# Kernel tuning notes

Hardware: AMD Instinct MI355X
Metric: run time of the kernel (lower is better)

## Reference

```python
import jax, jax.numpy as jnp
import numpy as np

T, A = 2048, 64          # n_thread, n_agents
RAWOB, N_TP, N_GP = 120, 5, 2
E = N_TP * N_GP          # number of sub-nets (type x group placeholder)
D = RAWOB + N_TP + 1     # augmented obs dim fed to each Net
H = 128                  # hidden width of each sub-net MLP
N_ACTION = 16


def setup_inputs() -> dict:
    key = jax.random.key(0)
    ks = jax.random.split(key, 12)
    s1 = 1.0 / np.sqrt(D)
    s2 = 1.0 / np.sqrt(H)
    return {
        "obs": jax.random.normal(ks[0], (T, A, RAWOB), dtype=jnp.float32),
        "hete_pick": jax.random.randint(ks[1], (T, A), 0, E),
        "hete_type": jax.random.randint(ks[2], (T, A), 0, N_TP),
        "gp_sel_summary": jax.random.randint(ks[3], (T, N_TP), 0, N_GP),
        # per-expert actor MLP params [E, ...]
        "W1": jax.random.normal(ks[4], (E, D, H), dtype=jnp.float32) * s1,
        "b1": jnp.zeros((E, H), dtype=jnp.float32),
        "W2": jax.random.normal(ks[5], (E, H, N_ACTION), dtype=jnp.float32) * s2,
        "b2": jnp.zeros((E, N_ACTION), dtype=jnp.float32),
        # central critic params
        "Wc1": jax.random.normal(ks[6], (D, H), dtype=jnp.float32) * s1,
        "bc1": jnp.zeros((H,), dtype=jnp.float32),
        "Wc2": jax.random.normal(ks[7], (H, 1), dtype=jnp.float32) * s2,
        "bc2": jnp.zeros((1,), dtype=jnp.float32),
    }


def _augment_obs(obs, hete_type, gp_sel_summary):
    # obs <- cat(obs, hete_type, gp_sel_summary with -1 scattered at own type idx)
    t, a, _ = obs.shape
    n_tp = gp_sel_summary.shape[1]
    gp = jnp.broadcast_to(gp_sel_summary[:, None, :].astype(obs.dtype), (t, a, n_tp))
    oh = jax.nn.one_hot(hete_type, n_tp, dtype=obs.dtype)
    gp_obs = gp * (1.0 - oh) - oh  # scatter -1 at index hete_type
    return jnp.concatenate([obs, hete_type[..., None].astype(obs.dtype), gp_obs], axis=-1)


def reference(obs, hete_pick, hete_type, gp_sel_summary,
              W1, b1, W2, b2, Wc1, bc1, Wc2, bc2):
    t, a, _ = obs.shape
    x = _augment_obs(obs, hete_type, gp_sel_summary)          # [T, A, D]
    xf = x.reshape(t * a, -1)                                  # [N, D]
    pick = hete_pick.reshape(t * a)                            # [N]
    n_exp = W1.shape[0]
    # dispatch: each token routed to exactly one sub-net; dense compute + masked combine
    logits = jnp.zeros((t * a, W2.shape[-1]), dtype=obs.dtype)
    for e in range(n_exp):  # small fixed expert loop
        y = jax.nn.relu(xf @ W1[e] + b1[e]) @ W2[e] + b2[e]    # [N, n_action]
        logits = jnp.where((pick == e)[:, None], y, logits)
    logits = logits.reshape(t, a, -1)
    # central critic on all tokens
    value = (jax.nn.relu(xf @ Wc1 + bc1) @ Wc2 + bc2).reshape(t, a, 1)
    return logits, value
```

## Files before the change

### kernel.cpp

```cpp
#include <hip/hip_runtime.h>
#include <hip/hip_bf16.h>

#define T_DIM   2048
#define A_DIM   64
#define N_TOK   (T_DIM * A_DIM)
#define RAWOB   120
#define N_TP    5
#define E_EXP   10
#define D_DIM   126
#define DP      128
#define H_DIM   128
#define N_ACT   16
#define CAP     14336
#define BTOK    256
#define MAXC    (CAP / BTOK)
#define LOGITS_SZ (N_TOK * N_ACT)

typedef __bf16 bh8 __attribute__((ext_vector_type(8)));
typedef ushort u16x8 __attribute__((ext_vector_type(8)));
typedef ushort u16x4 __attribute__((ext_vector_type(4)));
typedef short  s16x4 __attribute__((ext_vector_type(4)));
typedef float  f32x4 __attribute__((ext_vector_type(4)));

__device__ __forceinline__ f32x4 mfma16(bh8 a, bh8 b, f32x4 c) {
    return __builtin_amdgcn_mfma_f32_16x16x32_bf16(a, b, c, 0, 0, 0);
}
__device__ __forceinline__ f32x4 mfma16k16(s16x4 a, s16x4 b, f32x4 c) {
    return __builtin_amdgcn_mfma_f32_16x16x16bf16_1k(a, b, c, 0, 0, 0);
}

__device__ __forceinline__ ushort f2bf(float f) {
    unsigned x = __builtin_bit_cast(unsigned, f);
    unsigned r = (x + 0x7fffu + ((x >> 16) & 1u)) >> 16;
    return (ushort)r;
}

#define W1P_N (E_EXP * H_DIM * DP)
#define W2P_N (E_EXP * N_ACT * H_DIM)
#define WC1P_N (DP * DP)

#define PB_BLOCKS 252

__global__ __launch_bounds__(256) void prep_bucket_kernel(
    const float* __restrict__ W1, const float* __restrict__ W2,
    const float* __restrict__ Wc1, const float* __restrict__ b1,
    const float* __restrict__ bc1, const int* __restrict__ pick,
    int* __restrict__ counts, int* __restrict__ order,
    ushort* __restrict__ W1p, ushort* __restrict__ W2p, ushort* __restrict__ Wc1p)
{
    int bx = blockIdx.x, tid = threadIdx.x;
    if (bx < 44) {
        __shared__ ushort st[32][130];
        const float* src;
        const float* bias;
        ushort* dstbase;
        int kt;
        if (bx < 40) {
            int e = bx >> 2;
            kt = bx & 3;
            src = W1 + (e * D_DIM + kt * 32) * H_DIM;
            bias = b1 + e * H_DIM;
            dstbase = W1p + e * (H_DIM * DP);
        } else {
            kt = bx - 40;
            src = Wc1 + kt * 32 * H_DIM;
            bias = bc1;
            dstbase = Wc1p;
        }
        int dmax = D_DIM - kt * 32;
#pragma unroll
        for (int p = 0; p < 16; ++p) {
            int idx = p * 256 + tid;
            int dd = idx >> 7, n = idx & 127;
            float v;
            if (dd < dmax)                    v = src[dd * H_DIM + n];
            else if (kt == 3 && dd == 30)     v = bias[n];
            else                              v = 0.f;
            st[dd][n] = f2bf(v);
        }
        __syncthreads();
#pragma unroll
        for (int p = 0; p < 16; ++p) {
            int idx = p * 256 + tid;
            int dd = idx >> 7, n = idx & 127;
            dstbase[((n >> 4) * 4 + kt) * 512 + ((dd >> 3) * 16 + (n & 15)) * 8 + (dd & 7)]
                = st[dd][n];
        }
    } else if (bx < 124) {
        int i = (bx - 44) * 256 + tid;
        int e   = i >> 11;
        int rem = i & 2047;
        int kk  = rem >> 8;
        int idx = rem & 255;
        int l = idx >> 2, j = idx & 3;
        int lq = l >> 4, lm = l & 15;
        W2p[i] = f2bf(W2[(e * H_DIM + kk * 16 + lq * 4 + j) * N_ACT + lm]);
    } else {
        __shared__ int lc[E_EXP], lb[E_EXP], lcur[E_EXP];
        if (tid < E_EXP) { lc[tid] = 0; lcur[tid] = 0; }
        __syncthreads();
        int base = (bx - 124) * 1024;
        int e4[4];
#pragma unroll
        for (int it = 0; it < 4; ++it) {
            e4[it] = pick[base + it * 256 + tid];
            atomicAdd(&lc[e4[it]], 1);
        }
        __syncthreads();
        if (tid < E_EXP) lb[tid] = atomicAdd(&counts[tid * 16], lc[tid]);
        __syncthreads();
#pragma unroll
        for (int it = 0; it < 4; ++it) {
            int e = e4[it];
            int pos = lb[e] + atomicAdd(&lcur[e], 1);
            if (pos < CAP) order[e * CAP + pos] = base + it * 256 + tid;
        }
    }
}

__global__ __launch_bounds__(512, 6) void moe_kernel(
    const float* __restrict__ obs, const int* __restrict__ hete_type,
    const int* __restrict__ gp_sel,
    const float* __restrict__ b2, const float* __restrict__ bc2,
    const int* __restrict__ counts, const int* __restrict__ order,
    const ushort* __restrict__ W1p, const ushort* __restrict__ W2p,
    const ushort* __restrict__ Wc1p, const float* __restrict__ Wc2,
    float* __restrict__ out)
{
    __shared__ __align__(16) ushort wlds[18432];

    const int bx = blockIdx.x;
    const int e = bx % E_EXP;
    const int c = bx / E_EXP;
    const int cnt = counts[e * 16];
    const int start = c * BTOK;
    if (start >= cnt) return;

    const int tid = threadIdx.x;
    const int w = tid >> 6;
    const int base = start + w * 32;
    const int l = tid & 63;
    const int lm = l & 15;
    const int lq = l >> 4;

    {
        const u16x8* s1 = (const u16x8*)(const void*)(W1p + e * (H_DIM * DP));
        u16x8* d1 = (u16x8*)(void*)wlds;
#pragma unroll
        for (int p = 0; p < 4; ++p) d1[p * 512 + tid] = s1[p * 512 + tid];
        if (tid < 256)
            ((u16x8*)(void*)(wlds + 16384))[tid] =
                ((const u16x8*)(const void*)(W2p + e * 2048))[tid];
    }

    const int* ord_e = order + e * CAP;

    bh8 a[2][4];
    int tokm[2];
#pragma unroll
    for (int mt = 0; mt < 2; ++mt) {
        const int slot = min(base + mt * 16 + lm, cnt - 1);
        const int tok = ord_e[slot];
        tokm[mt] = tok;
        const float* orow = obs + tok * RAWOB;
#pragma unroll
        for (int kt = 0; kt < 3; ++kt) {
            const float* p = orow + kt * 32 + lq * 8;
            float4 u0 = *(const float4*)(const void*)p;
            float4 u1 = *(const float4*)(const void*)(p + 4);
            u16x8 t;
            t[0] = f2bf(u0.x); t[1] = f2bf(u0.y); t[2] = f2bf(u0.z); t[3] = f2bf(u0.w);
            t[4] = f2bf(u1.x); t[5] = f2bf(u1.y); t[6] = f2bf(u1.z); t[7] = f2bf(u1.w);
            a[mt][kt] = __builtin_bit_cast(bh8, t);
        }
        u16x8 t;
        if (lq < 3) {
            const float* p = orow + 96 + lq * 8;
            float4 u0 = *(const float4*)(const void*)p;
            float4 u1 = *(const float4*)(const void*)(p + 4);
            t[0] = f2bf(u0.x); t[1] = f2bf(u0.y); t[2] = f2bf(u0.z); t[3] = f2bf(u0.w);
            t[4] = f2bf(u1.x); t[5] = f2bf(u1.y); t[6] = f2bf(u1.z); t[7] = f2bf(u1.w);
        } else {
            int ht = hete_type[tok];
            int tt = tok >> 6;
            t[0] = f2bf((float)ht);
#pragma unroll
            for (int q = 0; q < N_TP; ++q) {
                float g = (q == ht) ? -1.0f : (float)gp_sel[tt * N_TP + q];
                t[1 + q] = f2bf(g);
            }
            t[6] = (ushort)0x3F80;
            t[7] = 0;
        }
        a[mt][3] = __builtin_bit_cast(bh8, t);
    }

    const float bb  = b2[e * N_ACT + lm];
    const float bcv = bc2[0];

    __syncthreads();

#pragma unroll
    for (int mt = 0; mt < 2; ++mt) {
        f32x4 y = (f32x4){0.f, 0.f, 0.f, 0.f};
#pragma unroll
        for (int nt = 0; nt < 8; ++nt) {
            f32x4 ae = (f32x4){0.f, 0.f, 0.f, 0.f};
#pragma unroll
            for (int kt = 0; kt < 4; ++kt) {
                bh8 wf = *(const bh8*)(const void*)(wlds + (nt * 4 + kt) * 512 + l * 8);
                ae = mfma16(wf, a[mt][kt], ae);
            }
            u16x4 hp;
            hp[0] = f2bf(fmaxf(ae[0], 0.f));
            hp[1] = f2bf(fmaxf(ae[1], 0.f));
            hp[2] = f2bf(fmaxf(ae[2], 0.f));
            hp[3] = f2bf(fmaxf(ae[3], 0.f));
            s16x4 w2f = *(const s16x4*)(const void*)(wlds + 16384 + nt * 256 + l * 4);
            y = mfma16k16(__builtin_bit_cast(s16x4, hp), w2f, y);
        }
#pragma unroll
        for (int r = 0; r < 4; ++r) {
            int m = mt * 16 + lq * 4 + r;
            if (base + m < cnt)
                out[ord_e[base + m] * N_ACT + lm] = y[r] + bb;
        }
    }

    {
        float p0 = 0.f, p1 = 0.f;
#pragma unroll
        for (int nt = 0; nt < 8; ++nt) {
            f32x4 c0 = (f32x4){0.f,0.f,0.f,0.f}, c1 = c0;
#pragma unroll
            for (int kt = 0; kt < 4; ++kt) {
                bh8 wf = *(const bh8*)(const void*)(Wc1p + (nt * 4 + kt) * 512 + l * 8);
                c0 = mfma16(wf, a[0][kt], c0);
                c1 = mfma16(wf, a[1][kt], c1);
            }
            const float4 wc = *(const float4*)(const void*)(Wc2 + nt * 16 + lq * 4);
            p0 += fmaxf(c0[0], 0.f) * wc.x + fmaxf(c0[1], 0.f) * wc.y
                + fmaxf(c0[2], 0.f) * wc.z + fmaxf(c0[3], 0.f) * wc.w;
            p1 += fmaxf(c1[0], 0.f) * wc.x + fmaxf(c1[1], 0.f) * wc.y
                + fmaxf(c1[2], 0.f) * wc.z + fmaxf(c1[3], 0.f) * wc.w;
        }
        p0 += __shfl_xor(p0, 16, 64); p0 += __shfl_xor(p0, 32, 64);
        p1 += __shfl_xor(p1, 16, 64); p1 += __shfl_xor(p1, 32, 64);
        if (lq == 0) {
            if (base + lm < cnt)      out[LOGITS_SZ + tokm[0]] = p0 + bcv;
            if (base + 16 + lm < cnt) out[LOGITS_SZ + tokm[1]] = p1 + bcv;
        }
    }
}

extern "C" void kernel_launch(void* const* d_in, const int* in_sizes, int n_in,
                              void* d_out, int out_size, void* d_ws, size_t ws_size,
                              hipStream_t stream) {
    const float* obs  = (const float*)d_in[0];
    const int*   pick = (const int*)d_in[1];
    const int*   htyp = (const int*)d_in[2];
    const int*   gp   = (const int*)d_in[3];
    const float* W1   = (const float*)d_in[4];
    const float* b1   = (const float*)d_in[5];
    const float* W2   = (const float*)d_in[6];
    const float* b2   = (const float*)d_in[7];
    const float* Wc1  = (const float*)d_in[8];
    const float* bc1  = (const float*)d_in[9];
    const float* Wc2  = (const float*)d_in[10];
    const float* bc2  = (const float*)d_in[11];
    float* out = (float*)d_out;

    int*    counts = (int*)d_ws;
    int*    order  = counts + 160;
    ushort* W1p    = (ushort*)(order + E_EXP * CAP);
    ushort* W2p    = W1p + W1P_N;
    ushort* Wc1p   = W2p + W2P_N;

    hipMemsetAsync(counts, 0, 160 * sizeof(int), stream);
    prep_bucket_kernel<<<PB_BLOCKS, 256, 0, stream>>>(
        W1, W2, Wc1, b1, bc1, pick, counts, order, W1p, W2p, Wc1p);
    moe_kernel<<<E_EXP * MAXC, 512, 0, stream>>>(
        obs, htyp, gp, b2, bc2, counts, order,
        W1p, W2p, Wc1p, Wc2, out);
}
```

Measured before the change: 142.4 us.

## Stage critic weights in LDS, sentinel-fill order buffer, interleave expert M-tiles

Copies the shared critic weight matrix into LDS alongside the expert weights, so the critic GEMM reads from LDS instead of global memory. Replaces per-bucket count checks with a 0xFF-memset order buffer whose -1 sentinels mark empty slots, which removes the counts read and the early exit. Blocks with empty buckets now still load weights and compute before discarding results. The bucketing blocks handle 4096 tokens each and reuse the local atomic return value as the slot offset, and the two M-tiles of the expert MLP are interleaved so MFMAs share weight fragments. The cost is double the LDS per block (which may reduce occupancy) plus an extra memset of the order array.

```diff
diff --git a/kernel.cpp b/kernel.cpp
--- a/kernel.cpp
+++ b/kernel.cpp
@@ -39,7 +39,11 @@
 #define W2P_N (E_EXP * N_ACT * H_DIM)
 #define WC1P_N (DP * DP)
 
-#define PB_BLOCKS 252
+#define LDS_W2  16384
+#define LDS_WC1 18432
+#define LDS_TOT 34816
+
+#define PB_BLOCKS 156
 
 __global__ __launch_bounds__(256) void prep_bucket_kernel(
     const float* __restrict__ W1, const float* __restrict__ W2,
@@ -96,23 +100,23 @@
         int lq = l >> 4, lm = l & 15;
         W2p[i] = f2bf(W2[(e * H_DIM + kk * 16 + lq * 4 + j) * N_ACT + lm]);
     } else {
-        __shared__ int lc[E_EXP], lb[E_EXP], lcur[E_EXP];
-        if (tid < E_EXP) { lc[tid] = 0; lcur[tid] = 0; }
-        __syncthreads();
-        int base = (bx - 124) * 1024;
-        int e4[4];
-#pragma unroll
-        for (int it = 0; it < 4; ++it) {
-            e4[it] = pick[base + it * 256 + tid];
-            atomicAdd(&lc[e4[it]], 1);
+        __shared__ int lc[E_EXP], lb[E_EXP];
+        if (tid < E_EXP) lc[tid] = 0;
+        __syncthreads();
+        int base = (bx - 124) * 4096;
+        int ev[16], loc[16];
+#pragma unroll
+        for (int it = 0; it < 16; ++it) {
+            ev[it] = pick[base + it * 256 + tid];
+            loc[it] = atomicAdd(&lc[ev[it]], 1);
         }
         __syncthreads();
         if (tid < E_EXP) lb[tid] = atomicAdd(&counts[tid * 16], lc[tid]);
         __syncthreads();
 #pragma unroll
-        for (int it = 0; it < 4; ++it) {
-            int e = e4[it];
-            int pos = lb[e] + atomicAdd(&lcur[e], 1);
+        for (int it = 0; it < 16; ++it) {
+            int e = ev[it];
+            int pos = lb[e] + loc[it];
             if (pos < CAP) order[e * CAP + pos] = base + it * 256 + tid;
         }
     }
@@ -122,45 +126,48 @@
     const float* __restrict__ obs, const int* __restrict__ hete_type,
     const int* __restrict__ gp_sel,
     const float* __restrict__ b2, const float* __restrict__ bc2,
-    const int* __restrict__ counts, const int* __restrict__ order,
+    const int* __restrict__ order,
     const ushort* __restrict__ W1p, const ushort* __restrict__ W2p,
     const ushort* __restrict__ Wc1p, const float* __restrict__ Wc2,
     float* __restrict__ out)
 {
-    __shared__ __align__(16) ushort wlds[18432];
+    __shared__ __align__(16) ushort wlds[LDS_TOT];
 
     const int bx = blockIdx.x;
     const int e = bx % E_EXP;
     const int c = bx / E_EXP;
-    const int cnt = counts[e * 16];
-    const int start = c * BTOK;
-    if (start >= cnt) return;
-
     const int tid = threadIdx.x;
     const int w = tid >> 6;
-    const int base = start + w * 32;
+    const int base = c * BTOK + w * 32;
     const int l = tid & 63;
     const int lm = l & 15;
     const int lq = l >> 4;
 
+    const int* ord_e = order + e * CAP;
+
+    int sraw[2];
+    sraw[0] = ord_e[base + lm];
+    sraw[1] = ord_e[base + 16 + lm];
+
     {
         const u16x8* s1 = (const u16x8*)(const void*)(W1p + e * (H_DIM * DP));
         u16x8* d1 = (u16x8*)(void*)wlds;
 #pragma unroll
         for (int p = 0; p < 4; ++p) d1[p * 512 + tid] = s1[p * 512 + tid];
+        const u16x8* sc = (const u16x8*)(const void*)Wc1p;
+        u16x8* dc = (u16x8*)(void*)(wlds + LDS_WC1);
+#pragma unroll
+        for (int p = 0; p < 4; ++p) dc[p * 512 + tid] = sc[p * 512 + tid];
         if (tid < 256)
-            ((u16x8*)(void*)(wlds + 16384))[tid] =
+            ((u16x8*)(void*)(wlds + LDS_W2))[tid] =
                 ((const u16x8*)(const void*)(W2p + e * 2048))[tid];
     }
-
-    const int* ord_e = order + e * CAP;
 
     bh8 a[2][4];
     int tokm[2];
 #pragma unroll
     for (int mt = 0; mt < 2; ++mt) {
-        const int slot = min(base + mt * 16 + lm, cnt - 1);
-        const int tok = ord_e[slot];
+        const int tok = sraw[mt] < 0 ? 0 : sraw[mt];
         tokm[mt] = tok;
         const float* orow = obs + tok * RAWOB;
 #pragma unroll
@@ -200,30 +207,34 @@
 
     __syncthreads();
 
-#pragma unroll
-    for (int mt = 0; mt < 2; ++mt) {
-        f32x4 y = (f32x4){0.f, 0.f, 0.f, 0.f};
+    {
+        f32x4 y0 = (f32x4){0.f, 0.f, 0.f, 0.f};
+        f32x4 y1 = (f32x4){0.f, 0.f, 0.f, 0.f};
 #pragma unroll
         for (int nt = 0; nt < 8; ++nt) {
-            f32x4 ae = (f32x4){0.f, 0.f, 0.f, 0.f};
+            f32x4 ae0 = (f32x4){0.f, 0.f, 0.f, 0.f}, ae1 = ae0;
 #pragma unroll
             for (int kt = 0; kt < 4; ++kt) {
                 bh8 wf = *(const bh8*)(const void*)(wlds + (nt * 4 + kt) * 512 + l * 8);
-                ae = mfma16(wf, a[mt][kt], ae);
-            }
-            u16x4 hp;
-            hp[0] = f2bf(fmaxf(ae[0], 0.f));
-            hp[1] = f2bf(fmaxf(ae[1], 0.f));
-            hp[2] = f2bf(fmaxf(ae[2], 0.f));
-            hp[3] = f2bf(fmaxf(ae[3], 0.f));
-            s16x4 w2f = *(const s16x4*)(const void*)(wlds + 16384 + nt * 256 + l * 4);
-            y = mfma16k16(__builtin_bit_cast(s16x4, hp), w2f, y);
+                ae0 = mfma16(wf, a[0][kt], ae0);
+                ae1 = mfma16(wf, a[1][kt], ae1);
+            }
+            u16x4 hp0, hp1;
+#pragma unroll
+            for (int r = 0; r < 4; ++r) {
+                hp0[r] = f2bf(fmaxf(ae0[r], 0.f));
+                hp1[r] = f2bf(fmaxf(ae1[r], 0.f));
+            }
+            s16x4 w2f = *(const s16x4*)(const void*)(wlds + LDS_W2 + nt * 256 + l * 4);
+            y0 = mfma16k16(__builtin_bit_cast(s16x4, hp0), w2f, y0);
+            y1 = mfma16k16(__builtin_bit_cast(s16x4, hp1), w2f, y1);
         }
 #pragma unroll
         for (int r = 0; r < 4; ++r) {
-            int m = mt * 16 + lq * 4 + r;
-            if (base + m < cnt)
-                out[ord_e[base + m] * N_ACT + lm] = y[r] + bb;
+            int s0 = ord_e[base + lq * 4 + r];
+            if (s0 >= 0) out[s0 * N_ACT + lm] = y0[r] + bb;
+            int s1 = ord_e[base + 16 + lq * 4 + r];
+            if (s1 >= 0) out[s1 * N_ACT + lm] = y1[r] + bb;
         }
     }
 
@@ -234,7 +245,8 @@
             f32x4 c0 = (f32x4){0.f,0.f,0.f,0.f}, c1 = c0;
 #pragma unroll
             for (int kt = 0; kt < 4; ++kt) {
-                bh8 wf = *(const bh8*)(const void*)(Wc1p + (nt * 4 + kt) * 512 + l * 8);
+                bh8 wf = *(const bh8*)(const void*)
+                         (wlds + LDS_WC1 + (nt * 4 + kt) * 512 + l * 8);
                 c0 = mfma16(wf, a[0][kt], c0);
                 c1 = mfma16(wf, a[1][kt], c1);
             }
@@ -247,8 +259,8 @@
         p0 += __shfl_xor(p0, 16, 64); p0 += __shfl_xor(p0, 32, 64);
         p1 += __shfl_xor(p1, 16, 64); p1 += __shfl_xor(p1, 32, 64);
         if (lq == 0) {
-            if (base + lm < cnt)      out[LOGITS_SZ + tokm[0]] = p0 + bcv;
-            if (base + 16 + lm < cnt) out[LOGITS_SZ + tokm[1]] = p1 + bcv;
+            if (sraw[0] >= 0) out[LOGITS_SZ + tokm[0]] = p0 + bcv;
+            if (sraw[1] >= 0) out[LOGITS_SZ + tokm[1]] = p1 + bcv;
         }
     }
 }
@@ -277,9 +289,10 @@
     ushort* Wc1p   = W2p + W2P_N;
 
     hipMemsetAsync(counts, 0, 160 * sizeof(int), stream);
+    hipMemsetAsync(order, 0xFF, E_EXP * CAP * sizeof(int), stream);
     prep_bucket_kernel<<<PB_BLOCKS, 256, 0, stream>>>(
         W1, W2, Wc1, b1, bc1, pick, counts, order, W1p, W2p, Wc1p);
     moe_kernel<<<E_EXP * MAXC, 512, 0, stream>>>(
-        obs, htyp, gp, b2, bc2, counts, order,
+        obs, htyp, gp, b2, bc2, order,
         W1p, W2p, Wc1p, Wc2, out);
 }
```

Result: faster. 139.3 us (-2.2%).

## Replace global expert bucketing with per-block local sort over contiguous token tiles

Applied to the files above, without the earlier changes.

Removes the global counting/scatter pass and the memset, so each block takes 256 contiguous tokens, stages their augmented bf16 features in swizzled LDS, and groups them by expert locally into 16-row tiles. Weights for each expert are now read directly from global memory (L2/L1) rather than staged in LDS, and the critic uses the same LDS tile. This drops a launch, the atomics and the scattered obs gathers, and gives coalesced obs loads. In exchange, tiles are padded per expert inside each block (up to 10 partial tiles), weight loads go through cache per wave, and occupancy drops because of the 64KB LDS buffer.

```diff
diff --git a/kernel.cpp b/kernel.cpp
--- a/kernel.cpp
+++ b/kernel.cpp
@@ -11,9 +11,8 @@
 #define DP      128
 #define H_DIM   128
 #define N_ACT   16
-#define CAP     14336
 #define BTOK    256
-#define MAXC    (CAP / BTOK)
+#define NBLK    (N_TOK / BTOK)
 #define LOGITS_SZ (N_TOK * N_ACT)
 
 typedef __bf16 bh8 __attribute__((ext_vector_type(8)));
@@ -39,13 +38,12 @@
 #define W2P_N (E_EXP * N_ACT * H_DIM)
 #define WC1P_N (DP * DP)
 
-#define PB_BLOCKS 252
-
-__global__ __launch_bounds__(256) void prep_bucket_kernel(
+#define PB_BLOCKS 124
+
+__global__ __launch_bounds__(256) void prep_kernel(
     const float* __restrict__ W1, const float* __restrict__ W2,
     const float* __restrict__ Wc1, const float* __restrict__ b1,
-    const float* __restrict__ bc1, const int* __restrict__ pick,
-    int* __restrict__ counts, int* __restrict__ order,
+    const float* __restrict__ bc1,
     ushort* __restrict__ W1p, ushort* __restrict__ W2p, ushort* __restrict__ Wc1p)
 {
     int bx = blockIdx.x, tid = threadIdx.x;
@@ -86,7 +84,7 @@
             dstbase[((n >> 4) * 4 + kt) * 512 + ((dd >> 3) * 16 + (n & 15)) * 8 + (dd & 7)]
                 = st[dd][n];
         }
-    } else if (bx < 124) {
+    } else {
         int i = (bx - 44) * 256 + tid;
         int e   = i >> 11;
         int rem = i & 2047;
@@ -95,139 +93,136 @@
         int l = idx >> 2, j = idx & 3;
         int lq = l >> 4, lm = l & 15;
         W2p[i] = f2bf(W2[(e * H_DIM + kk * 16 + lq * 4 + j) * N_ACT + lm]);
-    } else {
-        __shared__ int lc[E_EXP], lb[E_EXP], lcur[E_EXP];
-        if (tid < E_EXP) { lc[tid] = 0; lcur[tid] = 0; }
-        __syncthreads();
-        int base = (bx - 124) * 1024;
-        int e4[4];
-#pragma unroll
-        for (int it = 0; it < 4; ++it) {
-            e4[it] = pick[base + it * 256 + tid];
-            atomicAdd(&lc[e4[it]], 1);
-        }
-        __syncthreads();
-        if (tid < E_EXP) lb[tid] = atomicAdd(&counts[tid * 16], lc[tid]);
-        __syncthreads();
-#pragma unroll
-        for (int it = 0; it < 4; ++it) {
-            int e = e4[it];
-            int pos = lb[e] + atomicAdd(&lcur[e], 1);
-            if (pos < CAP) order[e * CAP + pos] = base + it * 256 + tid;
-        }
-    }
-}
-
-__global__ __launch_bounds__(512, 6) void moe_kernel(
-    const float* __restrict__ obs, const int* __restrict__ hete_type,
-    const int* __restrict__ gp_sel,
+    }
+}
+
+__global__ __launch_bounds__(512, 4) void moe_kernel(
+    const float* __restrict__ obs, const int* __restrict__ pick,
+    const int* __restrict__ hete_type, const int* __restrict__ gp_sel,
     const float* __restrict__ b2, const float* __restrict__ bc2,
-    const int* __restrict__ counts, const int* __restrict__ order,
     const ushort* __restrict__ W1p, const ushort* __restrict__ W2p,
     const ushort* __restrict__ Wc1p, const float* __restrict__ Wc2,
     float* __restrict__ out)
 {
-    __shared__ __align__(16) ushort wlds[18432];
-
-    const int bx = blockIdx.x;
-    const int e = bx % E_EXP;
-    const int c = bx / E_EXP;
-    const int cnt = counts[e * 16];
-    const int start = c * BTOK;
-    if (start >= cnt) return;
-
+    __shared__ __align__(16) ushort xa[BTOK * 128];
+    __shared__ short map[416];
+    __shared__ short texp[32];
+    __shared__ int lc[16], lbase[16];
+    __shared__ int nt_tot;
+
+    const int bx  = blockIdx.x;
     const int tid = threadIdx.x;
+    const int gbase = bx * BTOK;
+
+    if (tid < 16) lc[tid] = 0;
+    for (int i = tid; i < 416; i += 512) map[i] = -1;
+    __syncthreads();
+
+    int mye = 0, myloc = 0;
+    if (tid < 256) {
+        mye = pick[gbase + tid];
+        myloc = atomicAdd(&lc[mye], 1);
+    }
+
+#pragma unroll
+    for (int p = 0; p < 8; ++p) {
+        int idx = p * 512 + tid;
+        if (idx < 3840) {
+            int r = idx / 15, g = idx - r * 15;
+            const float* s = obs + (size_t)(gbase + r) * RAWOB + g * 8;
+            float4 u0 = *(const float4*)(const void*)s;
+            float4 u1 = *(const float4*)(const void*)(s + 4);
+            u16x8 t;
+            t[0] = f2bf(u0.x); t[1] = f2bf(u0.y); t[2] = f2bf(u0.z); t[3] = f2bf(u0.w);
+            t[4] = f2bf(u1.x); t[5] = f2bf(u1.y); t[6] = f2bf(u1.z); t[7] = f2bf(u1.w);
+            *(u16x8*)(void*)(xa + r * 128 + (g ^ (r & 15)) * 8) = t;
+        }
+    }
+    if (tid < 256) {
+        int tok = gbase + tid;
+        int ht = hete_type[tok];
+        int tt = tok >> 6;
+        u16x8 t;
+        t[0] = f2bf((float)ht);
+#pragma unroll
+        for (int q = 0; q < N_TP; ++q) {
+            float g = (q == ht) ? -1.0f : (float)gp_sel[tt * N_TP + q];
+            t[1 + q] = f2bf(g);
+        }
+        t[6] = (ushort)0x3F80;
+        t[7] = 0;
+        *(u16x8*)(void*)(xa + tid * 128 + (15 ^ (tid & 15)) * 8) = t;
+    }
+    __syncthreads();
+
+    if (tid == 0) {
+        int pb = 0, t = 0;
+#pragma unroll
+        for (int e = 0; e < E_EXP; ++e) {
+            lbase[e] = pb;
+            int nt = (lc[e] + 15) >> 4;
+            for (int k = 0; k < nt; ++k) texp[t++] = (short)e;
+            pb += nt << 4;
+        }
+        nt_tot = t;
+    }
+    __syncthreads();
+    if (tid < 256) map[lbase[mye] + myloc] = (short)tid;
+    __syncthreads();
+
     const int w = tid >> 6;
-    const int base = start + w * 32;
     const int l = tid & 63;
     const int lm = l & 15;
     const int lq = l >> 4;
-
-    {
-        const u16x8* s1 = (const u16x8*)(const void*)(W1p + e * (H_DIM * DP));
-        u16x8* d1 = (u16x8*)(void*)wlds;
-#pragma unroll
-        for (int p = 0; p < 4; ++p) d1[p * 512 + tid] = s1[p * 512 + tid];
-        if (tid < 256)
-            ((u16x8*)(void*)(wlds + 16384))[tid] =
-                ((const u16x8*)(const void*)(W2p + e * 2048))[tid];
-    }
-
-    const int* ord_e = order + e * CAP;
-
-    bh8 a[2][4];
-    int tokm[2];
-#pragma unroll
-    for (int mt = 0; mt < 2; ++mt) {
-        const int slot = min(base + mt * 16 + lm, cnt - 1);
-        const int tok = ord_e[slot];
-        tokm[mt] = tok;
-        const float* orow = obs + tok * RAWOB;
-#pragma unroll
-        for (int kt = 0; kt < 3; ++kt) {
-            const float* p = orow + kt * 32 + lq * 8;
-            float4 u0 = *(const float4*)(const void*)p;
-            float4 u1 = *(const float4*)(const void*)(p + 4);
-            u16x8 t;
-            t[0] = f2bf(u0.x); t[1] = f2bf(u0.y); t[2] = f2bf(u0.z); t[3] = f2bf(u0.w);
-            t[4] = f2bf(u1.x); t[5] = f2bf(u1.y); t[6] = f2bf(u1.z); t[7] = f2bf(u1.w);
-            a[mt][kt] = __builtin_bit_cast(bh8, t);
-        }
-        u16x8 t;
-        if (lq < 3) {
-            const float* p = orow + 96 + lq * 8;
-            float4 u0 = *(const float4*)(const void*)p;
-            float4 u1 = *(const float4*)(const void*)(p + 4);
-            t[0] = f2bf(u0.x); t[1] = f2bf(u0.y); t[2] = f2bf(u0.z); t[3] = f2bf(u0.w);
-            t[4] = f2bf(u1.x); t[5] = f2bf(u1.y); t[6] = f2bf(u1.z); t[7] = f2bf(u1.w);
-        } else {
-            int ht = hete_type[tok];
-            int tt = tok >> 6;
-            t[0] = f2bf((float)ht);
-#pragma unroll
-            for (int q = 0; q < N_TP; ++q) {
-                float g = (q == ht) ? -1.0f : (float)gp_sel[tt * N_TP + q];
-                t[1 + q] = f2bf(g);
-            }
-            t[6] = (ushort)0x3F80;
-            t[7] = 0;
-        }
-        a[mt][3] = __builtin_bit_cast(bh8, t);
-    }
-
-    const float bb  = b2[e * N_ACT + lm];
     const float bcv = bc2[0];
 
-    __syncthreads();
-
-#pragma unroll
-    for (int mt = 0; mt < 2; ++mt) {
+    const int NT = nt_tot;
+    for (int i = w; i < NT; i += 8) {
+        const int e  = texp[i];
+        const int tb = i << 4;
+        const int mlt = map[tb + lm];
+        const int row = mlt < 0 ? 0 : mlt;
+        bh8 a[4];
+#pragma unroll
+        for (int kt = 0; kt < 4; ++kt) {
+            int g = kt * 4 + lq;
+            a[kt] = *(const bh8*)(const void*)(xa + row * 128 + (g ^ (row & 15)) * 8);
+        }
+        const ushort* w1e = W1p + e * (H_DIM * DP);
+        const ushort* w2e = W2p + e * 2048;
+        const float bb = b2[e * N_ACT + lm];
         f32x4 y = (f32x4){0.f, 0.f, 0.f, 0.f};
 #pragma unroll
         for (int nt = 0; nt < 8; ++nt) {
             f32x4 ae = (f32x4){0.f, 0.f, 0.f, 0.f};
 #pragma unroll
             for (int kt = 0; kt < 4; ++kt) {
-                bh8 wf = *(const bh8*)(const void*)(wlds + (nt * 4 + kt) * 512 + l * 8);
-                ae = mfma16(wf, a[mt][kt], ae);
+                bh8 wf = *(const bh8*)(const void*)(w1e + (nt * 4 + kt) * 512 + l * 8);
+                ae = mfma16(wf, a[kt], ae);
             }
             u16x4 hp;
-            hp[0] = f2bf(fmaxf(ae[0], 0.f));
-            hp[1] = f2bf(fmaxf(ae[1], 0.f));
-            hp[2] = f2bf(fmaxf(ae[2], 0.f));
-            hp[3] = f2bf(fmaxf(ae[3], 0.f));
-            s16x4 w2f = *(const s16x4*)(const void*)(wlds + 16384 + nt * 256 + l * 4);
+#pragma unroll
+            for (int r = 0; r < 4; ++r) hp[r] = f2bf(fmaxf(ae[r], 0.f));
+            s16x4 w2f = *(const s16x4*)(const void*)(w2e + nt * 256 + l * 4);
             y = mfma16k16(__builtin_bit_cast(s16x4, hp), w2f, y);
         }
 #pragma unroll
         for (int r = 0; r < 4; ++r) {
-            int m = mt * 16 + lq * 4 + r;
-            if (base + m < cnt)
-                out[ord_e[base + m] * N_ACT + lm] = y[r] + bb;
+            int m2 = map[tb + lq * 4 + r];
+            if (m2 >= 0) out[(size_t)(gbase + m2) * N_ACT + lm] = y[r] + bb;
         }
     }
 
     {
+        const int r0 = w * 32;
+        const int row0 = r0 + lm, row1 = r0 + 16 + lm;
+        bh8 a0[4], a1[4];
+#pragma unroll
+        for (int kt = 0; kt < 4; ++kt) {
+            int g = kt * 4 + lq;
+            a0[kt] = *(const bh8*)(const void*)(xa + row0 * 128 + (g ^ (row0 & 15)) * 8);
+            a1[kt] = *(const bh8*)(const void*)(xa + row1 * 128 + (g ^ (row1 & 15)) * 8);
+        }
         float p0 = 0.f, p1 = 0.f;
 #pragma unroll
         for (int nt = 0; nt < 8; ++nt) {
@@ -235,8 +230,8 @@
 #pragma unroll
             for (int kt = 0; kt < 4; ++kt) {
                 bh8 wf = *(const bh8*)(const void*)(Wc1p + (nt * 4 + kt) * 512 + l * 8);
-                c0 = mfma16(wf, a[0][kt], c0);
-                c1 = mfma16(wf, a[1][kt], c1);
+                c0 = mfma16(wf, a0[kt], c0);
+                c1 = mfma16(wf, a1[kt], c1);
             }
             const float4 wc = *(const float4*)(const void*)(Wc2 + nt * 16 + lq * 4);
             p0 += fmaxf(c0[0], 0.f) * wc.x + fmaxf(c0[1], 0.f) * wc.y
@@ -247,8 +242,8 @@
         p0 += __shfl_xor(p0, 16, 64); p0 += __shfl_xor(p0, 32, 64);
         p1 += __shfl_xor(p1, 16, 64); p1 += __shfl_xor(p1, 32, 64);
         if (lq == 0) {
-            if (base + lm < cnt)      out[LOGITS_SZ + tokm[0]] = p0 + bcv;
-            if (base + 16 + lm < cnt) out[LOGITS_SZ + tokm[1]] = p1 + bcv;
+            out[LOGITS_SZ + gbase + row0] = p0 + bcv;
+            out[LOGITS_SZ + gbase + row1] = p1 + bcv;
         }
     }
 }
@@ -270,16 +265,13 @@
     const float* bc2  = (const float*)d_in[11];
     float* out = (float*)d_out;
 
-    int*    counts = (int*)d_ws;
-    int*    order  = counts + 160;
-    ushort* W1p    = (ushort*)(order + E_EXP * CAP);
-    ushort* W2p    = W1p + W1P_N;
-    ushort* Wc1p   = W2p + W2P_N;
-
-    hipMemsetAsync(counts, 0, 160 * sizeof(int), stream);
-    prep_bucket_kernel<<<PB_BLOCKS, 256, 0, stream>>>(
-        W1, W2, Wc1, b1, bc1, pick, counts, order, W1p, W2p, Wc1p);
-    moe_kernel<<<E_EXP * MAXC, 512, 0, stream>>>(
-        obs, htyp, gp, b2, bc2, counts, order,
+    ushort* W1p  = (ushort*)d_ws;
+    ushort* W2p  = W1p + W1P_N;
+    ushort* Wc1p = W2p + W2P_N;
+
+    prep_kernel<<<PB_BLOCKS, 256, 0, stream>>>(
+        W1, W2, Wc1, b1, bc1, W1p, W2p, Wc1p);
+    moe_kernel<<<NBLK, 512, 0, stream>>>(
+        obs, pick, htyp, gp, b2, bc2,
         W1p, W2p, Wc1p, Wc2, out);
 }
```

Result: faster. 137.2 us (-3.7%).
